# Optimization experiments

Hardware: AMD Instinct MI355X
Metric: run time of the kernel (lower is better)

## Reference

```python
import jax, jax.numpy as jnp
import numpy as np

B, C_IN, C_OUT, H, W, K = 8, 64, 64, 64, 64, 9
T = H * W  # 4096 tokens
EPS = 1e-12  # F.normalize eps


def setup_inputs() -> dict:
    key = jax.random.key(0)
    ks = jax.random.split(key, 7)
    x = jax.random.normal(ks[0], (B, C_IN, H, W), dtype=jnp.float32)
    Wq = jax.random.normal(ks[1], (T, T), dtype=jnp.float32) * 0.02
    Wk = jax.random.normal(ks[2], (T, T), dtype=jnp.float32) * 0.02
    Wv = jax.random.normal(ks[3], (T, T), dtype=jnp.float32) * 0.02
    Wo = jax.random.normal(ks[4], (T, T), dtype=jnp.float32) * 0.02
    conv_w = jax.random.normal(ks[5], (C_OUT, C_IN, K), dtype=jnp.float32) * 0.05
    conv_b = jax.random.normal(ks[6], (C_OUT,), dtype=jnp.float32) * 0.01
    return {"x": x, "Wq": Wq, "Wk": Wk, "Wv": Wv, "Wo": Wo,
            "conv_w": conv_w, "conv_b": conv_b}


def reference(x, Wq, Wk, Wv, Wo, conv_w, conv_b):
    Bq, Cc, Hh, Ww = x.shape
    Tt = Hh * Ww
    xf = x.reshape(Bq, Cc, Tt)  # flatten(start_dim=2)
    # nn.Linear over the token (last) dim: y[...,s] = sum_t x[...,t] * W[s,t]
    q = jnp.einsum('bct,st->bcs', xf, Wq)
    k = jnp.einsum('bct,st->bcs', xf, Wk)
    v = jnp.einsum('bct,st->bcs', xf, Wv)
    # cosine similarity over channel dim (dim=1), clamp to >= 0
    kn = k / jnp.maximum(jnp.linalg.norm(k, axis=1, keepdims=True), EPS)
    qn = q / jnp.maximum(jnp.linalg.norm(q, axis=1, keepdims=True), EPS)
    sim = jnp.clip(jnp.einsum('bct,bcs->bts', kn, qn), 0.0, None)  # [B,T,T]
    # top-K most similar neighbors per token (largest=True for similarity)
    _, idx = jax.lax.top_k(sim, K)  # [B,T,K] int32
    # gather neighbor values: prime[b,c,t,j] = v[b,c,idx[b,t,j]]
    gather = jax.vmap(lambda vv, ii: vv[:, ii])  # vv:[C,T], ii:[T,K] -> [C,T,K]
    prime = gather(v, idx).reshape(Bq, Cc, Tt * K)
    # Conv1d(kernel=K, stride=K, padding=0): aggregates each K-neighbor group
    out = jax.lax.conv_general_dilated(
        prime, conv_w, window_strides=(K,), padding='VALID',
        dimension_numbers=('NCH', 'OIH', 'NCH'))  # [B,C_OUT,T]
    out = out + conv_b[None, :, None]
    out = jnp.einsum('bct,st->bcs', out, Wo)  # w_o over token dim
    return out.reshape(Bq, conv_w.shape[0], Hh, Ww)
```

## Files before the change

### kernel.cpp

```cpp
#include <hip/hip_runtime.h>

#define T4096 4096
#define CH 64
typedef unsigned long long u64;

__global__ __launch_bounds__(256) void gemm_qkv(
    const float* __restrict__ X,
    const float* __restrict__ Wq, const float* __restrict__ Wk, const float* __restrict__ Wv,
    float* __restrict__ QT, float* __restrict__ KT, float* __restrict__ VT)
{
    const float* W = (blockIdx.z == 0) ? Wq : (blockIdx.z == 1) ? Wk : Wv;
    float*       O = (blockIdx.z == 0) ? QT : (blockIdx.z == 1) ? KT : VT;
    const int b  = blockIdx.y;
    const int s0 = blockIdx.x * 128;

    __shared__ float As[64][132];
    __shared__ float Bs[64][68];

    const int tid = threadIdx.x;
    const int tx = tid & 15;   const int c0 = tx * 4;
    const int my = tid >> 4;   const int m0 = my * 8;
    const int lr = tid >> 3;
    const int lk = (tid & 7) * 4;
    const int sw = lk;

    float acc[8][4];
#pragma unroll
    for (int i = 0; i < 8; ++i)
#pragma unroll
        for (int j = 0; j < 4; ++j) acc[i][j] = 0.f;

    const float* Xb = X + (size_t)b * CH * T4096;

    for (int k0 = 0; k0 < T4096; k0 += 64) {
#pragma unroll
        for (int kk = 0; kk < 2; ++kk) {
            const int kb = 32 * kk + lk;
#pragma unroll
            for (int p = 0; p < 4; ++p) {
                int row = lr + 32 * p;
                float4 v = *(const float4*)(W + (size_t)(s0 + row) * T4096 + k0 + kb);
                int col = row ^ sw;
                As[kb + 0][col] = v.x; As[kb + 1][col] = v.y;
                As[kb + 2][col] = v.z; As[kb + 3][col] = v.w;
            }
#pragma unroll
            for (int p = 0; p < 2; ++p) {
                int row = lr + 32 * p;
                float4 v = *(const float4*)(Xb + (size_t)row * T4096 + k0 + kb);
                int col = row ^ sw;
                Bs[kb + 0][col] = v.x; Bs[kb + 1][col] = v.y;
                Bs[kb + 2][col] = v.z; Bs[kb + 3][col] = v.w;
            }
        }
        __syncthreads();
#pragma unroll
        for (int k = 0; k < 64; ++k) {
            const int swk = k & 28;
            float4 a0 = *(const float4*)&As[k][(m0) ^ swk];
            float4 a1 = *(const float4*)&As[k][(m0 + 4) ^ swk];
            float4 bv = *(const float4*)&Bs[k][c0 ^ swk];
            float am[8] = {a0.x,a0.y,a0.z,a0.w,a1.x,a1.y,a1.z,a1.w};
            float bn[4] = {bv.x,bv.y,bv.z,bv.w};
#pragma unroll
            for (int i = 0; i < 8; ++i)
#pragma unroll
                for (int j = 0; j < 4; ++j) acc[i][j] = fmaf(am[i], bn[j], acc[i][j]);
        }
        __syncthreads();
    }
    if (blockIdx.z == 0) {
#pragma unroll
        for (int i = 0; i < 8; ++i) {
            int s = s0 + m0 + i;
            *(float4*)(O + ((((size_t)b * 64 + (s >> 6)) * 16 + tx) * 64 + (s & 63)) * 4) =
                make_float4(acc[i][0], acc[i][1], acc[i][2], acc[i][3]);
        }
    } else {
#pragma unroll
        for (int i = 0; i < 8; ++i) {
            *(float4*)(O + ((size_t)b * T4096 + s0 + m0 + i) * CH + c0) =
                make_float4(acc[i][0], acc[i][1], acc[i][2], acc[i][3]);
        }
    }
}

__global__ __launch_bounds__(256) void normalize_qk(float* __restrict__ QT, float* __restrict__ KT)
{
    int gtok = blockIdx.x * 4 + (threadIdx.x >> 6);
    int lane = threadIdx.x & 63;
    bool isQ = (gtok < 8 * T4096);
    int t = gtok & (T4096 - 1);
    int b = (gtok >> 12) & 7;
    float* p;
    if (isQ) p = QT + ((((size_t)b * 64 + (t >> 6)) * 16 + (lane >> 2)) * 64 + (t & 63)) * 4 + (lane & 3);
    else     p = KT + ((size_t)b * T4096 + t) * CH + lane;
    float v = *p;
    float ss = v * v;
#pragma unroll
    for (int off = 32; off; off >>= 1) ss += __shfl_xor(ss, off);
    float n = fmaxf(sqrtf(ss), 1e-12f);
    *p = v / n;
}

__global__ __launch_bounds__(512) void sim_topk(
    const float* __restrict__ Qr, const float* __restrict__ KT, int* __restrict__ IDX)
{
    const int wg = blockIdx.x;
    const int b  = wg & 7;
    const int t0 = (wg >> 3) * 32;

    __shared__ float Kn[32][68];

    const int tid = threadIdx.x;
    const int tx = tid & 31;
    const int ty = tid >> 5;

    {
        int row = tid >> 4; int cc = (tid & 15) * 4;
        *(float4*)&Kn[row][cc] =
            *(const float4*)(KT + ((size_t)b * T4096 + t0 + row) * CH + cc);
    }
    __syncthreads();

    u64 tv[2][9];
#pragma unroll
    for (int r = 0; r < 2; ++r)
#pragma unroll
        for (int q = 0; q < 9; ++q) tv[r][q] = 0ULL;
    u64 thr[2] = {0ULL, 0ULL};

    const float* qb0 = Qr + ((size_t)b * 64 * 1024 + tx) * 4;

    for (int blk = 0; blk < 64; ++blk) {
        const float* bp = qb0 + (size_t)blk * 4096;
        float acc[2][2];
        acc[0][0] = acc[0][1] = acc[1][0] = acc[1][1] = 0.f;

#pragma unroll 2
        for (int c4g = 0; c4g < 16; ++c4g) {
            float4 q0 = *(const float4*)(bp + c4g * 256);
            float4 q1 = *(const float4*)(bp + c4g * 256 + 128);
            float4 k0 = *(const float4*)&Kn[ty][c4g * 4];
            float4 k1 = *(const float4*)&Kn[16 + ty][c4g * 4];
            acc[0][0] = fmaf(k0.x, q0.x, acc[0][0]); acc[0][0] = fmaf(k0.y, q0.y, acc[0][0]);
            acc[0][0] = fmaf(k0.z, q0.z, acc[0][0]); acc[0][0] = fmaf(k0.w, q0.w, acc[0][0]);
            acc[0][1] = fmaf(k0.x, q1.x, acc[0][1]); acc[0][1] = fmaf(k0.y, q1.y, acc[0][1]);
            acc[0][1] = fmaf(k0.z, q1.z, acc[0][1]); acc[0][1] = fmaf(k0.w, q1.w, acc[0][1]);
            acc[1][0] = fmaf(k1.x, q0.x, acc[1][0]); acc[1][0] = fmaf(k1.y, q0.y, acc[1][0]);
            acc[1][0] = fmaf(k1.z, q0.z, acc[1][0]); acc[1][0] = fmaf(k1.w, q0.w, acc[1][0]);
            acc[1][1] = fmaf(k1.x, q1.x, acc[1][1]); acc[1][1] = fmaf(k1.y, q1.y, acc[1][1]);
            acc[1][1] = fmaf(k1.z, q1.z, acc[1][1]); acc[1][1] = fmaf(k1.w, q1.w, acc[1][1]);
        }

        bool ins = false;
        const int sb = blk * 64 + tx;
#pragma unroll
        for (int rr = 0; rr < 2; ++rr)
#pragma unroll
            for (int cc = 0; cc < 2; ++cc) {
                float v = fmaxf(acc[rr][cc], 0.f);
                int s = sb + 32 * cc;
                u64 key = ((u64)__float_as_uint(v) << 32) | (u64)(4095 - s);
                if (key > thr[rr]) {
                    u64 cv = key;
#pragma unroll
                    for (int p = 0; p < 9; ++p) {
                        u64 t  = tv[rr][p];
                        bool g = cv > t;
                        tv[rr][p] = g ? cv : t;
                        cv        = g ? t  : cv;
                    }
                    ins = true;
                }
            }
        if (__any(ins)) {
#pragma unroll
            for (int r = 0; r < 2; ++r) {
                u64 m = tv[r][8];
#pragma unroll
                for (int msk = 1; msk < 32; msk <<= 1) {
                    u64 o = __shfl_xor(m, msk);
                    if (o > m) m = o;
                }
                thr[r] = m;
            }
        }
    }

#pragma unroll
    for (int rr = 0; rr < 2; ++rr) {
        u64 mv[9];
#pragma unroll
        for (int q = 0; q < 9; ++q) mv[q] = tv[rr][q];
        const int outrow = t0 + rr * 16 + ty;
        int* dst = IDX + ((size_t)b * T4096 + outrow) * 9;
        for (int sel = 0; sel < 9; ++sel) {
            u64 bk = mv[0]; int bl = tx;
#pragma unroll
            for (int m = 1; m < 32; m <<= 1) {
                u64 ok = __shfl_xor(bk, m);
                int ol = __shfl_xor(bl, m);
                if (ok > bk) { bk = ok; bl = ol; }
            }
            if (tx == 0) dst[sel] = 4095 - (int)(unsigned)bk;
            if (tx == bl) {
#pragma unroll
                for (int q = 0; q < 8; ++q) mv[q] = mv[q + 1];
                mv[8] = 0ULL;
            }
        }
    }
}

__global__ void transpose_w(const float* __restrict__ cw, float* __restrict__ wT3)
{
    int idx = blockIdx.x * 256 + threadIdx.x;
    if (idx >= 64 * 64 * 9) return;
    int q   = idx & 3;
    int o   = (idx >> 2) & 63;
    int i4g = (idx >> 8) & 15;
    int j   = idx >> 12;
    wT3[idx] = cw[o * 576 + (i4g * 4 + q) * 9 + j];
}

__global__ __launch_bounds__(256) void gather_conv(
    const float* __restrict__ VT, const int* __restrict__ IDX,
    const float* __restrict__ wT3, const float* __restrict__ conv_b,
    float* __restrict__ out1)
{
    const int b  = blockIdx.y;
    const int w  = threadIdx.x >> 6;
    const int o  = threadIdx.x & 63;
    const int t0 = (blockIdx.x * 4 + w) * 4;

    __shared__ float vv[4][4][9][64];
    __shared__ int   nb[4][36];

    if (o < 36) nb[w][o] = IDX[((size_t)b * T4096 + t0) * 9 + o];
    __syncthreads();

#pragma unroll
    for (int tok = 0; tok < 4; ++tok)
#pragma unroll
        for (int j = 0; j < 9; ++j) {
            int n = nb[w][tok * 9 + j];
            vv[w][tok][j][o] = VT[((size_t)b * T4096 + n) * CH + o];
        }
    __syncthreads();

    float cb = conv_b[o];
    float a0 = cb, a1 = cb, a2 = cb, a3 = cb;
    for (int j = 0; j < 9; ++j) {
#pragma unroll
        for (int i4 = 0; i4 < 16; ++i4) {
            float4 w4 = *(const float4*)(wT3 + (((size_t)j * 16 + i4) * 64 + o) * 4);
            float4 v0 = *(const float4*)&vv[w][0][j][i4 * 4];
            float4 v1 = *(const float4*)&vv[w][1][j][i4 * 4];
            float4 v2 = *(const float4*)&vv[w][2][j][i4 * 4];
            float4 v3 = *(const float4*)&vv[w][3][j][i4 * 4];
            a0 = fmaf(v0.x, w4.x, a0); a0 = fmaf(v0.y, w4.y, a0); a0 = fmaf(v0.z, w4.z, a0); a0 = fmaf(v0.w, w4.w, a0);
            a1 = fmaf(v1.x, w4.x, a1); a1 = fmaf(v1.y, w4.y, a1); a1 = fmaf(v1.z, w4.z, a1); a1 = fmaf(v1.w, w4.w, a1);
            a2 = fmaf(v2.x, w4.x, a2); a2 = fmaf(v2.y, w4.y, a2); a2 = fmaf(v2.z, w4.z, a2); a2 = fmaf(v2.w, w4.w, a2);
            a3 = fmaf(v3.x, w4.x, a3); a3 = fmaf(v3.y, w4.y, a3); a3 = fmaf(v3.z, w4.z, a3); a3 = fmaf(v3.w, w4.w, a3);
        }
    }
    out1[((size_t)b * T4096 + t0 + 0) * CH + o] = a0;
    out1[((size_t)b * T4096 + t0 + 1) * CH + o] = a1;
    out1[((size_t)b * T4096 + t0 + 2) * CH + o] = a2;
    out1[((size_t)b * T4096 + t0 + 3) * CH + o] = a3;
}

__global__ __launch_bounds__(256) void gemm_out(
    const float* __restrict__ out1, const float* __restrict__ Wo, float* __restrict__ Out)
{
    const int b  = blockIdx.y;
    const int s0 = blockIdx.x * 128;
    __shared__ float As[32][68];
    __shared__ float Bs[32][132];
    const int tid = threadIdx.x;
    const int tx = tid & 15;  const int sl = tx * 8;
    const int my = tid >> 4;  const int c0 = my * 4;
    const int lr = tid >> 3;
    const int lk = (tid & 7) * 4;
    const int sw = lk;

    float acc[4][8];
#pragma unroll
    for (int i = 0; i < 4; ++i)
#pragma unroll
        for (int j = 0; j < 8; ++j) acc[i][j] = 0.f;

    for (int k0 = 0; k0 < T4096; k0 += 32) {
        {
            int r  = tid >> 3;
            int cL = (tid & 7) * 8;
            const float* src = out1 + ((size_t)b * T4096 + k0 + r) * CH + cL;
            *(float4*)&As[r][cL]     = *(const float4*)(src);
            *(float4*)&As[r][cL + 4] = *(const float4*)(src + 4);
        }
#pragma unroll
        for (int p = 0; p < 4; ++p) {
            int row = lr + 32 * p;
            float4 v = *(const float4*)(Wo + (size_t)(s0 + row) * T4096 + k0 + lk);
            int col = row ^ sw;
            Bs[lk + 0][col] = v.x; Bs[lk + 1][col] = v.y;
            Bs[lk + 2][col] = v.z; Bs[lk + 3][col] = v.w;
        }
        __syncthreads();
#pragma unroll
        for (int k = 0; k < 32; ++k) {
            const int swk = k & 28;
            float4 a  = *(const float4*)&As[k][c0];
            float4 b0 = *(const float4*)&Bs[k][(sl) ^ swk];
            float4 b1 = *(const float4*)&Bs[k][(sl + 4) ^ swk];
            float av[4] = {a.x, a.y, a.z, a.w};
            float bv[8] = {b0.x,b0.y,b0.z,b0.w,b1.x,b1.y,b1.z,b1.w};
#pragma unroll
            for (int i = 0; i < 4; ++i)
#pragma unroll
                for (int j = 0; j < 8; ++j) acc[i][j] = fmaf(av[i], bv[j], acc[i][j]);
        }
        __syncthreads();
    }
#pragma unroll
    for (int i = 0; i < 4; ++i) {
        float* dst = Out + ((size_t)b * CH + c0 + i) * T4096 + s0 + sl;
        *(float4*)dst       = make_float4(acc[i][0], acc[i][1], acc[i][2], acc[i][3]);
        *(float4*)(dst + 4) = make_float4(acc[i][4], acc[i][5], acc[i][6], acc[i][7]);
    }
}

extern "C" void kernel_launch(void* const* d_in, const int* in_sizes, int n_in,
                              void* d_out, int out_size, void* d_ws, size_t ws_size,
                              hipStream_t stream)
{
    const float* x  = (const float*)d_in[0];
    const float* Wq = (const float*)d_in[1];
    const float* Wk = (const float*)d_in[2];
    const float* Wv = (const float*)d_in[3];
    const float* Wo = (const float*)d_in[4];
    const float* cw = (const float*)d_in[5];
    const float* cb = (const float*)d_in[6];
    float* Out = (float*)d_out;

    char* ws = (char*)d_ws;
    float* QT   = (float*)(ws);
    float* KT   = (float*)(ws + (size_t)8  * 1024 * 1024);
    float* VT   = (float*)(ws + (size_t)16 * 1024 * 1024);
    int*   IDXb = (int*)  (ws + (size_t)24 * 1024 * 1024);
    float* wT3  = (float*)(ws + (size_t)26 * 1024 * 1024);
    float* out1 = QT;

    gemm_qkv<<<dim3(32, 8, 3), dim3(256), 0, stream>>>(x, Wq, Wk, Wv, QT, KT, VT);
    normalize_qk<<<dim3(16384), dim3(256), 0, stream>>>(QT, KT);
    sim_topk<<<dim3(1024), dim3(512), 0, stream>>>(QT, KT, IDXb);
    transpose_w<<<dim3(144), dim3(256), 0, stream>>>(cw, wT3);
    gather_conv<<<dim3(256, 8), dim3(256), 0, stream>>>(VT, IDXb, wT3, cb, out1);
    gemm_out<<<dim3(32, 8), dim3(256), 0, stream>>>(out1, Wo, Out);
}
```

Baseline: 1.742 ms.

## Double key rows per sim_topk block to reuse each Q load across four row groups

Each sim_topk block now handles 64 key tokens instead of 32. Every thread keeps four rows of accumulators and four top-9 lists, so each float4 of Q read from global memory feeds twice as many FMAs. The grid is halved to match. This roughly doubles per-thread register state (four u64 top-9 arrays), and the launch-bounds hint may push the compiler to spill. Fewer blocks also means less parallelism to hide latency.

```diff
diff --git a/kernel.cpp b/kernel.cpp
--- a/kernel.cpp
+++ b/kernel.cpp
@@ -103,60 +103,64 @@
     *p = v / n;
 }
 
-__global__ __launch_bounds__(512) void sim_topk(
+__global__ __launch_bounds__(512, 4) void sim_topk(
     const float* __restrict__ Qr, const float* __restrict__ KT, int* __restrict__ IDX)
 {
     const int wg = blockIdx.x;
     const int b  = wg & 7;
-    const int t0 = (wg >> 3) * 32;
-
-    __shared__ float Kn[32][68];
+    const int t0 = (wg >> 3) * 64;
+
+    __shared__ float Kn[64][68];
 
     const int tid = threadIdx.x;
     const int tx = tid & 31;
     const int ty = tid >> 5;
 
     {
-        int row = tid >> 4; int cc = (tid & 15) * 4;
-        *(float4*)&Kn[row][cc] =
-            *(const float4*)(KT + ((size_t)b * T4096 + t0 + row) * CH + cc);
+        int row = tid >> 3; int cc = (tid & 7) * 8;
+        const float* src = KT + ((size_t)b * T4096 + t0 + row) * CH + cc;
+        *(float4*)&Kn[row][cc]     = *(const float4*)(src);
+        *(float4*)&Kn[row][cc + 4] = *(const float4*)(src + 4);
     }
     __syncthreads();
 
-    u64 tv[2][9];
-#pragma unroll
-    for (int r = 0; r < 2; ++r)
+    u64 tv[4][9];
+#pragma unroll
+    for (int r = 0; r < 4; ++r)
 #pragma unroll
         for (int q = 0; q < 9; ++q) tv[r][q] = 0ULL;
-    u64 thr[2] = {0ULL, 0ULL};
+    u64 thr[4] = {0ULL, 0ULL, 0ULL, 0ULL};
 
     const float* qb0 = Qr + ((size_t)b * 64 * 1024 + tx) * 4;
 
     for (int blk = 0; blk < 64; ++blk) {
         const float* bp = qb0 + (size_t)blk * 4096;
-        float acc[2][2];
-        acc[0][0] = acc[0][1] = acc[1][0] = acc[1][1] = 0.f;
+        float acc[4][2];
+#pragma unroll
+        for (int r = 0; r < 4; ++r) { acc[r][0] = 0.f; acc[r][1] = 0.f; }
 
 #pragma unroll 2
         for (int c4g = 0; c4g < 16; ++c4g) {
             float4 q0 = *(const float4*)(bp + c4g * 256);
             float4 q1 = *(const float4*)(bp + c4g * 256 + 128);
-            float4 k0 = *(const float4*)&Kn[ty][c4g * 4];
-            float4 k1 = *(const float4*)&Kn[16 + ty][c4g * 4];
-            acc[0][0] = fmaf(k0.x, q0.x, acc[0][0]); acc[0][0] = fmaf(k0.y, q0.y, acc[0][0]);
-            acc[0][0] = fmaf(k0.z, q0.z, acc[0][0]); acc[0][0] = fmaf(k0.w, q0.w, acc[0][0]);
-            acc[0][1] = fmaf(k0.x, q1.x, acc[0][1]); acc[0][1] = fmaf(k0.y, q1.y, acc[0][1]);
-            acc[0][1] = fmaf(k0.z, q1.z, acc[0][1]); acc[0][1] = fmaf(k0.w, q1.w, acc[0][1]);
-            acc[1][0] = fmaf(k1.x, q0.x, acc[1][0]); acc[1][0] = fmaf(k1.y, q0.y, acc[1][0]);
-            acc[1][0] = fmaf(k1.z, q0.z, acc[1][0]); acc[1][0] = fmaf(k1.w, q0.w, acc[1][0]);
-            acc[1][1] = fmaf(k1.x, q1.x, acc[1][1]); acc[1][1] = fmaf(k1.y, q1.y, acc[1][1]);
-            acc[1][1] = fmaf(k1.z, q1.z, acc[1][1]); acc[1][1] = fmaf(k1.w, q1.w, acc[1][1]);
+            float4 kv[4];
+            kv[0] = *(const float4*)&Kn[ty][c4g * 4];
+            kv[1] = *(const float4*)&Kn[16 + ty][c4g * 4];
+            kv[2] = *(const float4*)&Kn[32 + ty][c4g * 4];
+            kv[3] = *(const float4*)&Kn[48 + ty][c4g * 4];
+#pragma unroll
+            for (int r = 0; r < 4; ++r) {
+                acc[r][0] = fmaf(kv[r].x, q0.x, acc[r][0]); acc[r][0] = fmaf(kv[r].y, q0.y, acc[r][0]);
+                acc[r][0] = fmaf(kv[r].z, q0.z, acc[r][0]); acc[r][0] = fmaf(kv[r].w, q0.w, acc[r][0]);
+                acc[r][1] = fmaf(kv[r].x, q1.x, acc[r][1]); acc[r][1] = fmaf(kv[r].y, q1.y, acc[r][1]);
+                acc[r][1] = fmaf(kv[r].z, q1.z, acc[r][1]); acc[r][1] = fmaf(kv[r].w, q1.w, acc[r][1]);
+            }
         }
 
         bool ins = false;
         const int sb = blk * 64 + tx;
 #pragma unroll
-        for (int rr = 0; rr < 2; ++rr)
+        for (int rr = 0; rr < 4; ++rr)
 #pragma unroll
             for (int cc = 0; cc < 2; ++cc) {
                 float v = fmaxf(acc[rr][cc], 0.f);
@@ -176,7 +180,7 @@
             }
         if (__any(ins)) {
 #pragma unroll
-            for (int r = 0; r < 2; ++r) {
+            for (int r = 0; r < 4; ++r) {
                 u64 m = tv[r][8];
 #pragma unroll
                 for (int msk = 1; msk < 32; msk <<= 1) {
@@ -189,7 +193,7 @@
     }
 
 #pragma unroll
-    for (int rr = 0; rr < 2; ++rr) {
+    for (int rr = 0; rr < 4; ++rr) {
         u64 mv[9];
 #pragma unroll
         for (int q = 0; q < 9; ++q) mv[q] = tv[rr][q];
@@ -354,7 +358,7 @@
 
     gemm_qkv<<<dim3(32, 8, 3), dim3(256), 0, stream>>>(x, Wq, Wk, Wv, QT, KT, VT);
     normalize_qk<<<dim3(16384), dim3(256), 0, stream>>>(QT, KT);
-    sim_topk<<<dim3(1024), dim3(512), 0, stream>>>(QT, KT, IDXb);
+    sim_topk<<<dim3(512), dim3(512), 0, stream>>>(QT, KT, IDXb);
     transpose_w<<<dim3(144), dim3(256), 0, stream>>>(cw, wT3);
     gather_conv<<<dim3(256, 8), dim3(256), 0, stream>>>(VT, IDXb, wT3, cb, out1);
     gemm_out<<<dim3(32, 8), dim3(256), 0, stream>>>(out1, Wo, Out);
```

New measurement: 1.740 ms. Within noise of the previous version (-0.2%).
